# Kernel tuning notes

Hardware: AMD Instinct MI355X
Metric: run time of the kernel (lower is better)

Reference implementation:

```python
import jax, jax.numpy as jnp
import numpy as np

N = 50000   # nodes
E = 600000  # edges (avg degree 12)
F = 16      # raw node features
P = 32      # n_channels_preproc
C = 128     # n_channels
L = 6       # n_gnn_layers
LBL = 2     # n_labels


def _dense_init(k, fan_in, shape):
    return (jax.random.normal(k, shape, jnp.float32) / np.float32(np.sqrt(fan_in)))


def setup_inputs() -> dict:
    key = jax.random.key(0)
    ks = jax.random.split(key, 12)
    return {
        "x": jax.random.normal(ks[0], (N, F), jnp.float32),
        "edge_src": jax.random.randint(ks[1], (E,), 0, N, dtype=jnp.int32),
        "edge_dst": jax.random.randint(ks[2], (E,), 0, N, dtype=jnp.int32),
        "edge_weight": jax.random.uniform(ks[3], (E,), jnp.float32),  # normalized-adjacency values
        "preproc_W": _dense_init(ks[4], F, (F, P)), "preproc_b": jnp.zeros((P,), jnp.float32),
        "fc_in1_W": _dense_init(ks[5], P, (P, C)), "fc_in1_b": jnp.zeros((C,), jnp.float32),
        "fc_in2_W": _dense_init(ks[6], P, (P, C)), "fc_in2_b": jnp.zeros((C,), jnp.float32),
        "gcn_W": _dense_init(ks[7], C, (L, C, C)), "gcn_b": jnp.zeros((L, C), jnp.float32),
        "fcg_W": _dense_init(ks[8], 2 * C, (L, 2 * C, C)), "fcg_b": jnp.zeros((L, C), jnp.float32),
        "last1_W": _dense_init(ks[9], 2 * C, (2 * C, C)), "last1_b": jnp.zeros((C,), jnp.float32),
        "last2_W": _dense_init(ks[10], C, (C, LBL)), "last2_b": jnp.zeros((LBL,), jnp.float32),
    }


def reference(x, edge_src, edge_dst, edge_weight,
              preproc_W, preproc_b, fc_in1_W, fc_in1_b, fc_in2_W, fc_in2_b,
              gcn_W, gcn_b, fcg_W, fcg_b, last1_W, last1_b, last2_W, last2_b):
    relu = jax.nn.relu
    h = relu(x @ preproc_W + preproc_b)                      # preproc Dense
    node_id = relu(h @ fc_in1_W + fc_in1_b)                  # node identity branch
    h = relu(h @ fc_in2_W + fc_in2_b)

    def layer(h, params):
        W, b, Wf, bf = params
        # GCNConv: act(A_hat @ (h @ W) + b), A_hat as COO edge list
        hw = h @ W                                           # [N, C]
        msg = hw[edge_src] * edge_weight[:, None]            # [E, C]
        agg = jax.ops.segment_sum(msg, edge_dst, num_segments=N)
        g = relu(agg + b)
        merged = jnp.concatenate([node_id, g], axis=-1)      # [N, 2C]
        return relu(merged @ Wf + bf), None                  # dropout = identity (eval)

    h, _ = jax.lax.scan(layer, h, (gcn_W, gcn_b, fcg_W, fcg_b))

    merged = jnp.concatenate([node_id, h], axis=-1)
    h = relu(merged @ last1_W + last1_b)
    return jax.nn.sigmoid(h @ last2_W + last2_b)             # [N, n_labels]
```

## Files before the change

kernel.cpp:

```cpp
#include <hip/hip_runtime.h>
#include <cstddef>
#include <cstdint>

#define NN 50000
#define NE 600000
#define SCAN_BLOCKS ((NN + 1023) / 1024)

typedef __attribute__((ext_vector_type(8))) short bf16x8;
typedef __attribute__((ext_vector_type(4))) float f32x4;

#define SWZ(x) (((x) ^ ((x) >> 2)) & 3)

__device__ __forceinline__ float bf2f(ushort u) {
    return __uint_as_float(((uint32_t)u) << 16);
}
__device__ __forceinline__ ushort f2bf(float f) {
    uint32_t b = __float_as_uint(f);
    return (ushort)((b + 0x7FFF + ((b >> 16) & 1)) >> 16);
}

__global__ __launch_bounds__(256)
void convert_weights(const float* __restrict__ f1W, const float* __restrict__ f2W,
                     const float* __restrict__ gW, const float* __restrict__ fgW,
                     const float* __restrict__ l1W, ushort* __restrict__ wt)
{
    int i = blockIdx.x * 256 + threadIdx.x;
    if (i >= 335872) return;
    float v;
    if (i < 4096) {
        int c = i >> 5, k = i & 31;
        v = f1W[k * 128 + c];
    } else if (i < 8192) {
        int j = i - 4096; int c = j >> 5, k = j & 31;
        v = f2W[k * 128 + c];
    } else if (i < 8192 + 98304) {
        int j = i - 8192; int l = j >> 14, r = j & 16383;
        int c = r >> 7, k = r & 127;
        v = gW[l * 16384 + k * 128 + c];
    } else if (i < 8192 + 98304 + 196608) {
        int j = i - (8192 + 98304); int l = j >> 15, r = j & 32767;
        int c = r >> 8, k = r & 255;
        v = fgW[l * 32768 + k * 128 + c];
    } else {
        int j = i - (8192 + 98304 + 196608);
        int c = j >> 8, k = j & 255;
        v = l1W[k * 128 + c];
    }
    wt[i] = f2bf(v);
}

__global__ __launch_bounds__(256)
void preproc_kernel(const float* __restrict__ x, const float* __restrict__ W,
                    const float* __restrict__ b, ushort* __restrict__ out)
{
    __shared__ float Wl[512];
    __shared__ float bl[32];
    int tx = threadIdx.x;
    Wl[tx]       = W[tx];
    Wl[tx + 256] = W[tx + 256];
    if (tx < 32) bl[tx] = b[tx];
    __syncthreads();
    int n = blockIdx.x * 256 + tx;
    if (n >= NN) return;
    float xr[16];
    const float4* xp = (const float4*)(x + (size_t)n * 16);
#pragma unroll
    for (int q = 0; q < 4; ++q) {
        float4 v = xp[q];
        xr[q*4+0]=v.x; xr[q*4+1]=v.y; xr[q*4+2]=v.z; xr[q*4+3]=v.w;
    }
    float acc[32];
#pragma unroll
    for (int c = 0; c < 32; ++c) acc[c] = bl[c];
#pragma unroll
    for (int k = 0; k < 16; ++k)
#pragma unroll
        for (int c = 0; c < 32; ++c)
            acc[c] = fmaf(xr[k], Wl[k*32+c], acc[c]);
    ushort4* op = (ushort4*)(out + (size_t)n * 32);
#pragma unroll
    for (int q = 0; q < 8; ++q) {
        ushort4 v;
        v.x = f2bf(fmaxf(acc[q*4+0], 0.f));
        v.y = f2bf(fmaxf(acc[q*4+1], 0.f));
        v.z = f2bf(fmaxf(acc[q*4+2], 0.f));
        v.w = f2bf(fmaxf(acc[q*4+3], 0.f));
        op[q] = v;
    }
}

__global__ __launch_bounds__(128)
void gemm_mfma(const ushort* __restrict__ A1, int K1,
               const ushort* __restrict__ Wt, const float* __restrict__ bias,
               ushort* __restrict__ out, int nrows)
{
    __shared__ ushort Atile[64 * 32];
    __shared__ ushort Btile[128 * 32];
    const int tx   = threadIdx.x;
    const int wave = tx >> 6;
    const int lane = tx & 63;
    const int bm   = blockIdx.x * 64;
    const int Ktot = K1;

    const int rs  = lane >> 2;
    const int chn = (lane & 3) ^ SWZ(rs);
    const int m    = lane & 15;
    const int quad = lane >> 4;
    const int slot = quad ^ SWZ(m);

    f32x4 acc0[8], acc1[8];
#pragma unroll
    for (int t = 0; t < 8; ++t) {
        acc0[t] = (f32x4){0.f, 0.f, 0.f, 0.f};
        acc1[t] = (f32x4){0.f, 0.f, 0.f, 0.f};
    }

    for (int kk = 0; kk < Ktot; kk += 32) {
#pragma unroll
        for (int i = 0; i < 2; ++i) {
            int seg = wave + 2 * i;
            int row = seg * 16 + rs;
            int ar  = bm + row; if (ar >= nrows) ar = nrows - 1;
            __builtin_amdgcn_global_load_lds(
                (const __attribute__((address_space(1))) void*)
                    (A1 + (size_t)ar * K1 + kk + chn * 8),
                (__attribute__((address_space(3))) void*)(Atile + seg * 512),
                16, 0, 0);
        }
#pragma unroll
        for (int i = 0; i < 4; ++i) {
            int seg = wave + 2 * i;
            int col = seg * 16 + rs;
            __builtin_amdgcn_global_load_lds(
                (const __attribute__((address_space(1))) void*)
                    (Wt + (size_t)col * Ktot + kk + chn * 8),
                (__attribute__((address_space(3))) void*)(Btile + seg * 512),
                16, 0, 0);
        }
        __syncthreads();
        bf16x8 af0 = *(const bf16x8*)(Atile + (wave * 32 + m) * 32 + slot * 8);
        bf16x8 af1 = *(const bf16x8*)(Atile + (wave * 32 + 16 + m) * 32 + slot * 8);
#pragma unroll
        for (int t = 0; t < 8; ++t) {
            bf16x8 bfr = *(const bf16x8*)(Btile + (t * 16 + m) * 32 + slot * 8);
            acc0[t] = __builtin_amdgcn_mfma_f32_16x16x32_bf16(af0, bfr, acc0[t], 0, 0, 0);
            acc1[t] = __builtin_amdgcn_mfma_f32_16x16x32_bf16(af1, bfr, acc1[t], 0, 0, 0);
        }
        __syncthreads();
    }

#pragma unroll
    for (int half = 0; half < 2; ++half) {
        const int orow0 = bm + wave * 32 + half * 16 + quad * 4;
#pragma unroll
        for (int t = 0; t < 8; ++t) {
            int col = t * 16 + m;
            float bb = bias[col];
            f32x4 a = half ? acc1[t] : acc0[t];
#pragma unroll
            for (int r = 0; r < 4; ++r) {
                int row = orow0 + r;
                if (row < nrows)
                    out[(size_t)row * 128 + col] = f2bf(fmaxf(a[r] + bb, 0.f));
            }
        }
    }
}

__global__ __launch_bounds__(128)
void gemm_fused(const ushort* __restrict__ A1, int K1,
                const ushort* __restrict__ A2, int K2,
                const ushort* __restrict__ Wt, const float* __restrict__ bias,
                const ushort* __restrict__ Wg,
                ushort* __restrict__ out_hw, int nrows)
{
    __shared__ ushort Atile[64 * 32];
    __shared__ ushort Btile[128 * 32];
    __shared__ ushort Xt[64 * 128];
    const int tx   = threadIdx.x;
    const int wave = tx >> 6;
    const int lane = tx & 63;
    const int bm   = blockIdx.x * 64;
    const int Ktot = K1 + K2;

    const int rs  = lane >> 2;
    const int chn = (lane & 3) ^ SWZ(rs);
    const int m    = lane & 15;
    const int quad = lane >> 4;
    const int slot = quad ^ SWZ(m);

    f32x4 acc0[8], acc1[8];
#pragma unroll
    for (int t = 0; t < 8; ++t) {
        acc0[t] = (f32x4){0.f, 0.f, 0.f, 0.f};
        acc1[t] = (f32x4){0.f, 0.f, 0.f, 0.f};
    }

    for (int kk = 0; kk < Ktot; kk += 32) {
        const ushort* asrc; int astr, kl;
        if (kk < K1) { asrc = A1; astr = K1; kl = kk; }
        else         { asrc = A2; astr = K2; kl = kk - K1; }
#pragma unroll
        for (int i = 0; i < 2; ++i) {
            int seg = wave + 2 * i;
            int row = seg * 16 + rs;
            int ar  = bm + row; if (ar >= nrows) ar = nrows - 1;
            __builtin_amdgcn_global_load_lds(
                (const __attribute__((address_space(1))) void*)
                    (asrc + (size_t)ar * astr + kl + chn * 8),
                (__attribute__((address_space(3))) void*)(Atile + seg * 512),
                16, 0, 0);
        }
#pragma unroll
        for (int i = 0; i < 4; ++i) {
            int seg = wave + 2 * i;
            int col = seg * 16 + rs;
            __builtin_amdgcn_global_load_lds(
                (const __attribute__((address_space(1))) void*)
                    (Wt + (size_t)col * Ktot + kk + chn * 8),
                (__attribute__((address_space(3))) void*)(Btile + seg * 512),
                16, 0, 0);
        }
        __syncthreads();
        bf16x8 af0 = *(const bf16x8*)(Atile + (wave * 32 + m) * 32 + slot * 8);
        bf16x8 af1 = *(const bf16x8*)(Atile + (wave * 32 + 16 + m) * 32 + slot * 8);
#pragma unroll
        for (int t = 0; t < 8; ++t) {
            bf16x8 bfr = *(const bf16x8*)(Btile + (t * 16 + m) * 32 + slot * 8);
            acc0[t] = __builtin_amdgcn_mfma_f32_16x16x32_bf16(af0, bfr, acc0[t], 0, 0, 0);
            acc1[t] = __builtin_amdgcn_mfma_f32_16x16x32_bf16(af1, bfr, acc1[t], 0, 0, 0);
        }
        __syncthreads();
    }

#pragma unroll
    for (int half = 0; half < 2; ++half) {
        int rbase = wave * 32 + half * 16 + quad * 4;
#pragma unroll
        for (int t = 0; t < 8; ++t) {
            int col = t * 16 + m;
            float bb = bias[col];
            int c32 = col >> 5, within = col & 7, ks = (col >> 3) & 3;
            f32x4 a = half ? acc1[t] : acc0[t];
#pragma unroll
            for (int r = 0; r < 4; ++r) {
                int row = rbase + r;
                int pos = ks ^ SWZ(row & 15);
                Xt[row * 128 + c32 * 32 + pos * 8 + within] =
                    f2bf(fmaxf(a[r] + bb, 0.f));
            }
        }
    }
#pragma unroll
    for (int t = 0; t < 8; ++t) {
        acc0[t] = (f32x4){0.f, 0.f, 0.f, 0.f};
        acc1[t] = (f32x4){0.f, 0.f, 0.f, 0.f};
    }
    __syncthreads();

    for (int c32 = 0; c32 < 4; ++c32) {
        int kk = c32 * 32;
#pragma unroll
        for (int i = 0; i < 4; ++i) {
            int seg = wave + 2 * i;
            int col = seg * 16 + rs;
            __builtin_amdgcn_global_load_lds(
                (const __attribute__((address_space(1))) void*)
                    (Wg + (size_t)col * 128 + kk + chn * 8),
                (__attribute__((address_space(3))) void*)(Btile + seg * 512),
                16, 0, 0);
        }
        __syncthreads();
        bf16x8 af0 = *(const bf16x8*)(Xt + (wave * 32 + m) * 128 + kk + slot * 8);
        bf16x8 af1 = *(const bf16x8*)(Xt + (wave * 32 + 16 + m) * 128 + kk + slot * 8);
#pragma unroll
        for (int t = 0; t < 8; ++t) {
            bf16x8 bfr = *(const bf16x8*)(Btile + (t * 16 + m) * 32 + slot * 8);
            acc0[t] = __builtin_amdgcn_mfma_f32_16x16x32_bf16(af0, bfr, acc0[t], 0, 0, 0);
            acc1[t] = __builtin_amdgcn_mfma_f32_16x16x32_bf16(af1, bfr, acc1[t], 0, 0, 0);
        }
        __syncthreads();
    }

#pragma unroll
    for (int half = 0; half < 2; ++half) {
        const int orow0 = bm + wave * 32 + half * 16 + quad * 4;
#pragma unroll
        for (int t = 0; t < 8; ++t) {
            int col = t * 16 + m;
            f32x4 a = half ? acc1[t] : acc0[t];
#pragma unroll
            for (int r = 0; r < 4; ++r) {
                int row = orow0 + r;
                if (row < nrows)
                    out_hw[(size_t)row * 128 + col] = f2bf(a[r]);
            }
        }
    }
}

__global__ __launch_bounds__(128)
void gemm_last(const ushort* __restrict__ nid, const ushort* __restrict__ agg,
               const ushort* __restrict__ Wt, const float* __restrict__ bias5,
               const ushort* __restrict__ Wl1, const float* __restrict__ l1b,
               const float* __restrict__ l2W, const float* __restrict__ l2b,
               float* __restrict__ out, int nrows)
{
    __shared__ ushort Atile[64 * 32];
    __shared__ ushort Btile[128 * 32];
    __shared__ ushort Xt[64 * 128];
    __shared__ float  w2s[256];
    const int tx   = threadIdx.x;
    const int wave = tx >> 6;
    const int lane = tx & 63;
    const int bm   = blockIdx.x * 64;

    w2s[tx]       = l2W[tx];
    w2s[tx + 128] = l2W[tx + 128];

    const int rs  = lane >> 2;
    const int chn = (lane & 3) ^ SWZ(rs);
    const int m    = lane & 15;
    const int quad = lane >> 4;
    const int slot = quad ^ SWZ(m);

    f32x4 acc0[8], acc1[8];
#pragma unroll
    for (int t = 0; t < 8; ++t) {
        acc0[t] = (f32x4){0.f, 0.f, 0.f, 0.f};
        acc1[t] = (f32x4){0.f, 0.f, 0.f, 0.f};
    }

    for (int kk = 0; kk < 256; kk += 32) {
        const ushort* asrc; int kl;
        if (kk < 128) { asrc = nid; kl = kk; }
        else          { asrc = agg; kl = kk - 128; }
#pragma unroll
        for (int i = 0; i < 2; ++i) {
            int seg = wave + 2 * i;
            int row = seg * 16 + rs;
            int ar  = bm + row; if (ar >= nrows) ar = nrows - 1;
            __builtin_amdgcn_global_load_lds(
                (const __attribute__((address_space(1))) void*)
                    (asrc + (size_t)ar * 128 + kl + chn * 8),
                (__attribute__((address_space(3))) void*)(Atile + seg * 512),
                16, 0, 0);
        }
#pragma unroll
        for (int i = 0; i < 4; ++i) {
            int seg = wave + 2 * i;
            int col = seg * 16 + rs;
            __builtin_amdgcn_global_load_lds(
                (const __attribute__((address_space(1))) void*)
                    (Wt + (size_t)col * 256 + kk + chn * 8),
                (__attribute__((address_space(3))) void*)(Btile + seg * 512),
                16, 0, 0);
        }
        __syncthreads();
        bf16x8 af0 = *(const bf16x8*)(Atile + (wave * 32 + m) * 32 + slot * 8);
        bf16x8 af1 = *(const bf16x8*)(Atile + (wave * 32 + 16 + m) * 32 + slot * 8);
#pragma unroll
        for (int t = 0; t < 8; ++t) {
            bf16x8 bfr = *(const bf16x8*)(Btile + (t * 16 + m) * 32 + slot * 8);
            acc0[t] = __builtin_amdgcn_mfma_f32_16x16x32_bf16(af0, bfr, acc0[t], 0, 0, 0);
            acc1[t] = __builtin_amdgcn_mfma_f32_16x16x32_bf16(af1, bfr, acc1[t], 0, 0, 0);
        }
        __syncthreads();
    }

#pragma unroll
    for (int half = 0; half < 2; ++half) {
        int rbase = wave * 32 + half * 16 + quad * 4;
#pragma unroll
        for (int t = 0; t < 8; ++t) {
            int col = t * 16 + m;
            float bb = bias5[col];
            int c32 = col >> 5, within = col & 7, ks = (col >> 3) & 3;
            f32x4 a = half ? acc1[t] : acc0[t];
#pragma unroll
            for (int r = 0; r < 4; ++r) {
                int row = rbase + r;
                int pos = ks ^ SWZ(row & 15);
                Xt[row * 128 + c32 * 32 + pos * 8 + within] =
                    f2bf(fmaxf(a[r] + bb, 0.f));
            }
        }
    }
#pragma unroll
    for (int t = 0; t < 8; ++t) {
        acc0[t] = (f32x4){0.f, 0.f, 0.f, 0.f};
        acc1[t] = (f32x4){0.f, 0.f, 0.f, 0.f};
    }
    __syncthreads();

    for (int c8 = 0; c8 < 8; ++c8) {
        int kk = c8 * 32;
        if (c8 < 4) {
#pragma unroll
            for (int i = 0; i < 2; ++i) {
                int seg = wave + 2 * i;
                int row = seg * 16 + rs;
                int ar  = bm + row; if (ar >= nrows) ar = nrows - 1;
                __builtin_amdgcn_global_load_lds(
                    (const __attribute__((address_space(1))) void*)
                        (nid + (size_t)ar * 128 + kk + chn * 8),
                    (__attribute__((address_space(3))) void*)(Atile + seg * 512),
                    16, 0, 0);
            }
        }
#pragma unroll
        for (int i = 0; i < 4; ++i) {
            int seg = wave + 2 * i;
            int col = seg * 16 + rs;
            __builtin_amdgcn_global_load_lds(
                (const __attribute__((address_space(1))) void*)
                    (Wl1 + (size_t)col * 256 + kk + chn * 8),
                (__attribute__((address_space(3))) void*)(Btile + seg * 512),
                16, 0, 0);
        }
        __syncthreads();
        bf16x8 af0, af1;
        if (c8 < 4) {
            af0 = *(const bf16x8*)(Atile + (wave * 32 + m) * 32 + slot * 8);
            af1 = *(const bf16x8*)(Atile + (wave * 32 + 16 + m) * 32 + slot * 8);
        } else {
            int ko = (c8 - 4) * 32;
            af0 = *(const bf16x8*)(Xt + (wave * 32 + m) * 128 + ko + slot * 8);
            af1 = *(const bf16x8*)(Xt + (wave * 32 + 16 + m) * 128 + ko + slot * 8);
        }
#pragma unroll
        for (int t = 0; t < 8; ++t) {
            bf16x8 bfr = *(const bf16x8*)(Btile + (t * 16 + m) * 32 + slot * 8);
            acc0[t] = __builtin_amdgcn_mfma_f32_16x16x32_bf16(af0, bfr, acc0[t], 0, 0, 0);
            acc1[t] = __builtin_amdgcn_mfma_f32_16x16x32_bf16(af1, bfr, acc1[t], 0, 0, 0);
        }
        __syncthreads();
    }

    float bb[8];
#pragma unroll
    for (int t = 0; t < 8; ++t) bb[t] = l1b[t * 16 + m];
    float b20 = l2b[0], b21 = l2b[1];
#pragma unroll
    for (int half = 0; half < 2; ++half) {
#pragma unroll
        for (int r = 0; r < 4; ++r) {
            float p0 = 0.f, p1 = 0.f;
#pragma unroll
            for (int t = 0; t < 8; ++t) {
                int col = t * 16 + m;
                f32x4 a = half ? acc1[t] : acc0[t];
                float v = fmaxf(a[r] + bb[t], 0.f);
                p0 = fmaf(v, w2s[col * 2 + 0], p0);
                p1 = fmaf(v, w2s[col * 2 + 1], p1);
            }
#pragma unroll
            for (int mask = 1; mask < 16; mask <<= 1) {
                p0 += __shfl_xor(p0, mask);
                p1 += __shfl_xor(p1, mask);
            }
            if (m == 0) {
                int row = bm + wave * 32 + half * 16 + quad * 4 + r;
                if (row < nrows) {
                    out[(size_t)row * 2 + 0] = 1.f / (1.f + __expf(-(p0 + b20)));
                    out[(size_t)row * 2 + 1] = 1.f / (1.f + __expf(-(p1 + b21)));
                }
            }
        }
    }
}

__global__ __launch_bounds__(256)
void hist_kernel(const int* __restrict__ dst, int* __restrict__ deg)
{
    int e = blockIdx.x * 256 + threadIdx.x;
    if (e < NE) atomicAdd(&deg[dst[e]], 1);
}

__global__ __launch_bounds__(1024)
void scan1_kernel(const int* __restrict__ deg, int* __restrict__ off,
                  int* __restrict__ bsum)
{
    __shared__ int buf[1024];
    int tx = threadIdx.x;
    int i = blockIdx.x * 1024 + tx;
    int v = (i < NN) ? deg[i] : 0;
    buf[tx] = v;
    __syncthreads();
    for (int s = 1; s < 1024; s <<= 1) {
        int t = (tx >= s) ? buf[tx - s] : 0;
        __syncthreads();
        buf[tx] += t;
        __syncthreads();
    }
    if (i < NN) off[i] = buf[tx] - v;
    if (tx == 1023) bsum[blockIdx.x] = buf[1023];
}

__global__ __launch_bounds__(64)
void scan2_kernel(int* __restrict__ bsum)
{
    __shared__ int buf[64];
    int tx = threadIdx.x;
    int v = (tx < SCAN_BLOCKS) ? bsum[tx] : 0;
    buf[tx] = v;
    __syncthreads();
    for (int s = 1; s < 64; s <<= 1) {
        int t = (tx >= s) ? buf[tx - s] : 0;
        __syncthreads();
        buf[tx] += t;
        __syncthreads();
    }
    if (tx < SCAN_BLOCKS) bsum[tx] = buf[tx] - v;
}

__global__ __launch_bounds__(1024)
void scan3_kernel(int* __restrict__ off, const int* __restrict__ bsum)
{
    int i = blockIdx.x * 1024 + threadIdx.x;
    if (i < NN) off[i] += bsum[blockIdx.x];
    if (i == 0) off[NN] = NE;
}

__global__ __launch_bounds__(256)
void permute_kernel(const int* __restrict__ src, const int* __restrict__ dst,
                    const float* __restrict__ w, const int* __restrict__ off,
                    int* __restrict__ cursor, unsigned int* __restrict__ esw)
{
    int e = blockIdx.x * 256 + threadIdx.x;
    if (e >= NE) return;
    int d = dst[e];
    int p = off[d] + atomicAdd(&cursor[d], 1);
    unsigned int packed = (unsigned int)src[e] |
                          ((unsigned int)f2bf(w[e]) << 17);
    __builtin_nontemporal_store(packed, &esw[p]);
}

__global__ __launch_bounds__(256)
void gather_agg(const ushort* __restrict__ hw,
                const unsigned int* __restrict__ esw,
                const int* __restrict__ off, const float* __restrict__ gbias,
                ushort* __restrict__ agg)
{
    const int g    = blockIdx.x * 4 + (threadIdx.x >> 6);
    const int lane = threadIdx.x & 63;
    int n = g * 8;
    if (n >= NN) return;
    int n_end = n + 8; if (n_end > NN) n_end = NN;
    const int base = off[n];
    const int end  = off[n_end];
    int nb = off[n + 1];
    const ushort* hp = hw + lane * 2;
    const float g0 = gbias[lane * 2], g1 = gbias[lane * 2 + 1];
    float a0 = 0.f, a1 = 0.f;

    for (int chunk = base; chunk < end; chunk += 64) {
        int idx = chunk + lane;
        int pk = (idx < end) ? (int)esw[idx] : 0;
        int cnt = end - chunk; if (cnt > 64) cnt = 64;
        int cnt8 = (cnt + 7) & ~7;
        for (int j = 0; j < cnt8; j += 8) {
            int pp[8];
            unsigned int rv[8];
#pragma unroll
            for (int k = 0; k < 8; ++k)
                pp[k] = __builtin_amdgcn_readlane(pk, j + k);
#pragma unroll
            for (int k = 0; k < 8; ++k)
                rv[k] = *(const unsigned int*)(hp + (size_t)(pp[k] & 0x1FFFF) * 128);
#pragma unroll
            for (int k = 0; k < 8; ++k) {
                int e = chunk + j + k;
                while (e == nb) {
                    unsigned int o = (unsigned int)f2bf(fmaxf(a0 + g0, 0.f)) |
                                     ((unsigned int)f2bf(fmaxf(a1 + g1, 0.f)) << 16);
                    *(unsigned int*)(agg + (size_t)n * 128 + lane * 2) = o;
                    a0 = 0.f; a1 = 0.f;
                    ++n;
                    nb = (n < n_end) ? off[n + 1] : 0x7fffffff;
                }
                float w = bf2f((ushort)((unsigned int)pp[k] >> 17));
                a0 = fmaf(bf2f((ushort)(rv[k] & 0xffff)), w, a0);
                a1 = fmaf(bf2f((ushort)(rv[k] >> 16)),    w, a1);
            }
        }
    }
    while (n < n_end) {
        unsigned int o = (unsigned int)f2bf(fmaxf(a0 + g0, 0.f)) |
                         ((unsigned int)f2bf(fmaxf(a1 + g1, 0.f)) << 16);
        *(unsigned int*)(agg + (size_t)n * 128 + lane * 2) = o;
        a0 = 0.f; a1 = 0.f;
        ++n;
    }
}

extern "C" void kernel_launch(void* const* d_in, const int* in_sizes, int n_in,
                              void* d_out, int out_size, void* d_ws, size_t ws_size,
                              hipStream_t stream)
{
    const float* x    = (const float*)d_in[0];
    const int*   esrc = (const int*)  d_in[1];
    const int*   edst = (const int*)  d_in[2];
    const float* ew   = (const float*)d_in[3];
    const float* preW = (const float*)d_in[4];
    const float* preb = (const float*)d_in[5];
    const float* f1W  = (const float*)d_in[6];
    const float* f1b  = (const float*)d_in[7];
    const float* f2W  = (const float*)d_in[8];
    const float* f2b  = (const float*)d_in[9];
    const float* gW   = (const float*)d_in[10];
    const float* gb   = (const float*)d_in[11];
    const float* fgW  = (const float*)d_in[12];
    const float* fgb  = (const float*)d_in[13];
    const float* l1W  = (const float*)d_in[14];
    const float* l1b  = (const float*)d_in[15];
    const float* l2W  = (const float*)d_in[16];
    const float* l2b  = (const float*)d_in[17];
    float* out = (float*)d_out;

    ushort* wt   = (ushort*)d_ws;
    ushort* wf1  = wt;
    ushort* wf2  = wf1 + 4096;
    ushort* wg   = wf2 + 4096;
    ushort* wfg  = wg  + 98304;
    ushort* wl1  = wfg + 196608;
    ushort* h0b  = wl1 + 32768;
    ushort* nidb = h0b  + (size_t)NN * 32;
    ushort* hwb  = nidb + (size_t)NN * 128;
    ushort* aggb = hwb  + (size_t)NN * 128;
    ushort* endu = aggb + (size_t)NN * 128;
    unsigned int* esw = (unsigned int*)(((uintptr_t)endu + 15) & ~(uintptr_t)15);
    int*   deg   = (int*)(esw + NE);
    int*   off   = deg + NN;
    int*   cursor= off + NN + 1;
    int*   bsum  = cursor + NN;

    const int gblocks = (NN + 63) / 64;
    const int eblocks = (NE + 255) / 256;
    const int ngroups = (NN + 7) / 8;
    const int wblocks = (ngroups + 3) / 4;

    convert_weights<<<(335872 + 255) / 256, 256, 0, stream>>>(f1W, f2W, gW, fgW, l1W, wt);

    hipMemsetAsync(deg, 0, (size_t)NN * sizeof(int), stream);
    hipMemsetAsync(cursor, 0, (size_t)NN * sizeof(int), stream);
    hist_kernel<<<eblocks, 256, 0, stream>>>(edst, deg);
    scan1_kernel<<<SCAN_BLOCKS, 1024, 0, stream>>>(deg, off, bsum);
    scan2_kernel<<<1, 64, 0, stream>>>(bsum);
    scan3_kernel<<<SCAN_BLOCKS, 1024, 0, stream>>>(off, bsum);
    permute_kernel<<<eblocks, 256, 0, stream>>>(esrc, edst, ew, off, cursor, esw);

    preproc_kernel<<<(NN + 255) / 256, 256, 0, stream>>>(x, preW, preb, h0b);
    gemm_mfma<<<gblocks, 128, 0, stream>>>(h0b, 32, wf1, f1b, nidb, NN);
    gemm_fused<<<gblocks, 128, 0, stream>>>(h0b, 32, nullptr, 0, wf2, f2b,
                                            wg, hwb, NN);
    for (int l = 0; l < 6; ++l) {
        gather_agg<<<wblocks, 256, 0, stream>>>(hwb, esw, off,
                                                gb + (size_t)l * 128, aggb);
        if (l < 5) {
            gemm_fused<<<gblocks, 128, 0, stream>>>(nidb, 128, aggb, 128,
                                                    wfg + (size_t)l * 32768,
                                                    fgb + (size_t)l * 128,
                                                    wg + (size_t)(l + 1) * 16384,
                                                    hwb, NN);
        }
    }
    gemm_last<<<gblocks, 128, 0, stream>>>(nidb, aggb,
                                           wfg + (size_t)5 * 32768,
                                           fgb + (size_t)5 * 128,
                                           wl1, l1b, l2W, l2b, out, NN);
}
```

Before: 451.8 us.

## Build CSR via two-pass bucketed counting sort with shared-memory histograms

```diff
diff --git a/kernel.cpp b/kernel.cpp
--- a/kernel.cpp
+++ b/kernel.cpp
@@ -4,7 +4,7 @@
 
 #define NN 50000
 #define NE 600000
-#define SCAN_BLOCKS ((NN + 1023) / 1024)
+#define NB 391
 
 typedef __attribute__((ext_vector_type(8))) short bf16x8;
 typedef __attribute__((ext_vector_type(4))) float f32x4;
@@ -470,70 +470,123 @@
     }
 }
 
+
 __global__ __launch_bounds__(256)
-void hist_kernel(const int* __restrict__ dst, int* __restrict__ deg)
-{
-    int e = blockIdx.x * 256 + threadIdx.x;
-    if (e < NE) atomicAdd(&deg[dst[e]], 1);
-}
-
-__global__ __launch_bounds__(1024)
-void scan1_kernel(const int* __restrict__ deg, int* __restrict__ off,
-                  int* __restrict__ bsum)
-{
-    __shared__ int buf[1024];
+void bhist_kernel(const int* __restrict__ dst, int* __restrict__ bcnt)
+{
+    __shared__ int h[NB];
     int tx = threadIdx.x;
-    int i = blockIdx.x * 1024 + tx;
-    int v = (i < NN) ? deg[i] : 0;
-    buf[tx] = v;
-    __syncthreads();
-    for (int s = 1; s < 1024; s <<= 1) {
-        int t = (tx >= s) ? buf[tx - s] : 0;
-        __syncthreads();
-        buf[tx] += t;
-        __syncthreads();
-    }
-    if (i < NN) off[i] = buf[tx] - v;
-    if (tx == 1023) bsum[blockIdx.x] = buf[1023];
-}
-
-__global__ __launch_bounds__(64)
-void scan2_kernel(int* __restrict__ bsum)
-{
-    __shared__ int buf[64];
+    for (int i = tx; i < NB; i += 256) h[i] = 0;
+    __syncthreads();
+    int e0 = blockIdx.x * 1024;
+#pragma unroll
+    for (int k = 0; k < 4; ++k) {
+        int e = e0 + k * 256 + tx;
+        if (e < NE) atomicAdd(&h[dst[e] >> 7], 1);
+    }
+    __syncthreads();
+    for (int i = tx; i < NB; i += 256)
+        if (h[i]) atomicAdd(&bcnt[i], h[i]);
+}
+
+__global__ __launch_bounds__(512)
+void bscan_kernel(const int* __restrict__ bcnt, int* __restrict__ bbase,
+                  int* __restrict__ bcur)
+{
+    __shared__ int buf[512];
+    int t = threadIdx.x;
+    int v = (t < NB) ? bcnt[t] : 0;
+    buf[t] = v;
+    __syncthreads();
+    for (int s = 1; s < 512; s <<= 1) {
+        int u = (t >= s) ? buf[t - s] : 0;
+        __syncthreads();
+        buf[t] += u;
+        __syncthreads();
+    }
+    if (t < NB) {
+        int ex = buf[t] - v;
+        bbase[t] = ex;
+        bcur[t]  = ex;
+    }
+    if (t == 0) bbase[NB] = NE;
+}
+
+__global__ __launch_bounds__(256)
+void pass1_kernel(const int* __restrict__ src, const int* __restrict__ dst,
+                  const float* __restrict__ w, int* __restrict__ bcur,
+                  unsigned int* __restrict__ stage_pk,
+                  unsigned char* __restrict__ stage_dl)
+{
+    __shared__ int cnt[NB];
+    __shared__ int gbase[NB];
     int tx = threadIdx.x;
-    int v = (tx < SCAN_BLOCKS) ? bsum[tx] : 0;
-    buf[tx] = v;
-    __syncthreads();
-    for (int s = 1; s < 64; s <<= 1) {
-        int t = (tx >= s) ? buf[tx - s] : 0;
-        __syncthreads();
-        buf[tx] += t;
-        __syncthreads();
-    }
-    if (tx < SCAN_BLOCKS) bsum[tx] = buf[tx] - v;
-}
-
-__global__ __launch_bounds__(1024)
-void scan3_kernel(int* __restrict__ off, const int* __restrict__ bsum)
-{
-    int i = blockIdx.x * 1024 + threadIdx.x;
-    if (i < NN) off[i] += bsum[blockIdx.x];
-    if (i == 0) off[NN] = NE;
+    for (int i = tx; i < NB; i += 256) cnt[i] = 0;
+    __syncthreads();
+    int e0 = blockIdx.x * 1024;
+    int myd[4], myrank[4];
+    unsigned int mypk[4];
+#pragma unroll
+    for (int k = 0; k < 4; ++k) {
+        int e = e0 + k * 256 + tx;
+        if (e < NE) {
+            int d = dst[e];
+            myd[k]    = d;
+            mypk[k]   = (unsigned int)src[e] | ((unsigned int)f2bf(w[e]) << 17);
+            myrank[k] = atomicAdd(&cnt[d >> 7], 1);
+        } else {
+            myd[k] = -1;
+        }
+    }
+    __syncthreads();
+    for (int i = tx; i < NB; i += 256)
+        gbase[i] = cnt[i] ? atomicAdd(&bcur[i], cnt[i]) : 0;
+    __syncthreads();
+#pragma unroll
+    for (int k = 0; k < 4; ++k) {
+        if (myd[k] >= 0) {
+            int p = gbase[myd[k] >> 7] + myrank[k];
+            stage_pk[p] = mypk[k];
+            stage_dl[p] = (unsigned char)(myd[k] & 127);
+        }
+    }
 }
 
 __global__ __launch_bounds__(256)
-void permute_kernel(const int* __restrict__ src, const int* __restrict__ dst,
-                    const float* __restrict__ w, const int* __restrict__ off,
-                    int* __restrict__ cursor, unsigned int* __restrict__ esw)
-{
-    int e = blockIdx.x * 256 + threadIdx.x;
-    if (e >= NE) return;
-    int d = dst[e];
-    int p = off[d] + atomicAdd(&cursor[d], 1);
-    unsigned int packed = (unsigned int)src[e] |
-                          ((unsigned int)f2bf(w[e]) << 17);
-    __builtin_nontemporal_store(packed, &esw[p]);
+void pass2_kernel(const unsigned int* __restrict__ stage_pk,
+                  const unsigned char* __restrict__ stage_dl,
+                  const int* __restrict__ bbase,
+                  unsigned int* __restrict__ esw, int* __restrict__ off)
+{
+    __shared__ int h[128];
+    __shared__ int lofs[128];
+    int b    = blockIdx.x;
+    int tx   = threadIdx.x;
+    int base = bbase[b];
+    int cnt  = bbase[b + 1] - base;
+    if (tx < 128) h[tx] = 0;
+    __syncthreads();
+    for (int i = tx; i < cnt; i += 256)
+        atomicAdd(&h[stage_dl[base + i]], 1);
+    __syncthreads();
+    if (tx == 0) {
+        int run = 0;
+        for (int i = 0; i < 128; ++i) { lofs[i] = run; run += h[i]; }
+    }
+    __syncthreads();
+    int node0 = b * 128;
+    if (tx < 128) {
+        int n = node0 + tx;
+        if (n < NN) off[n] = base + lofs[tx];
+        h[tx] = 0;
+    }
+    if (b == NB - 1 && tx == 0) off[NN] = NE;
+    __syncthreads();
+    for (int i = tx; i < cnt; i += 256) {
+        int d = stage_dl[base + i];
+        int r = atomicAdd(&h[d], 1);
+        esw[base + lofs[d] + r] = stage_pk[base + i];
+    }
 }
 
 __global__ __launch_bounds__(256)
@@ -629,26 +682,26 @@
     ushort* hwb  = nidb + (size_t)NN * 128;
     ushort* aggb = hwb  + (size_t)NN * 128;
     ushort* endu = aggb + (size_t)NN * 128;
-    unsigned int* esw = (unsigned int*)(((uintptr_t)endu + 15) & ~(uintptr_t)15);
-    int*   deg   = (int*)(esw + NE);
-    int*   off   = deg + NN;
-    int*   cursor= off + NN + 1;
-    int*   bsum  = cursor + NN;
+    unsigned int* esw      = (unsigned int*)(((uintptr_t)endu + 15) & ~(uintptr_t)15);
+    unsigned int* stage_pk = esw + NE;
+    int*          bcnt     = (int*)(stage_pk + NE);
+    int*          bbase    = bcnt + NB + 1;
+    int*          bcur     = bbase + NB + 1;
+    int*          off      = bcur + NB + 1;
+    unsigned char* stage_dl = (unsigned char*)(off + NN + 2);
 
     const int gblocks = (NN + 63) / 64;
-    const int eblocks = (NE + 255) / 256;
+    const int eblocks = (NE + 1023) / 1024;
     const int ngroups = (NN + 7) / 8;
     const int wblocks = (ngroups + 3) / 4;
 
     convert_weights<<<(335872 + 255) / 256, 256, 0, stream>>>(f1W, f2W, gW, fgW, l1W, wt);
 
-    hipMemsetAsync(deg, 0, (size_t)NN * sizeof(int), stream);
-    hipMemsetAsync(cursor, 0, (size_t)NN * sizeof(int), stream);
-    hist_kernel<<<eblocks, 256, 0, stream>>>(edst, deg);
-    scan1_kernel<<<SCAN_BLOCKS, 1024, 0, stream>>>(deg, off, bsum);
-    scan2_kernel<<<1, 64, 0, stream>>>(bsum);
-    scan3_kernel<<<SCAN_BLOCKS, 1024, 0, stream>>>(off, bsum);
-    permute_kernel<<<eblocks, 256, 0, stream>>>(esrc, edst, ew, off, cursor, esw);
+    hipMemsetAsync(bcnt, 0, (size_t)NB * sizeof(int), stream);
+    bhist_kernel<<<eblocks, 256, 0, stream>>>(edst, bcnt);
+    bscan_kernel<<<1, 512, 0, stream>>>(bcnt, bbase, bcur);
+    pass1_kernel<<<eblocks, 256, 0, stream>>>(esrc, edst, ew, bcur, stage_pk, stage_dl);
+    pass2_kernel<<<NB, 256, 0, stream>>>(stage_pk, stage_dl, bbase, esw, off);
 
     preproc_kernel<<<(NN + 255) / 256, 256, 0, stream>>>(x, preW, preb, h0b);
     gemm_mfma<<<gblocks, 128, 0, stream>>>(h0b, 32, wf1, f1b, nidb, NN);
```

Measured after the change: 428.1 us. 1.06x faster.
